# Kernel tuning notes

Measured on AMD Instinct MI355X. Metric: run time of the kernel, lower is better.

The kernel has to match this reference:

```python
import jax, jax.numpy as jnp
import numpy as np

B, C, D, H, W = 8, 256, 128, 64, 64


def setup_inputs() -> dict:
    key = jax.random.key(0)
    ks = jax.random.split(key, 7)
    s = 1.0 / np.sqrt(C)
    return {
        "q": jax.random.normal(ks[0], (B, C, H, W), dtype=jnp.float32),
        "k": jax.random.normal(ks[1], (B, C, H, W), dtype=jnp.float32),
        "v": jax.random.normal(ks[2], (B, C, H, W), dtype=jnp.float32),
        "W_theta": jax.random.normal(ks[3], (D, C), dtype=jnp.float32) * s,
        "W_phi": jax.random.normal(ks[4], (D, C), dtype=jnp.float32) * s,
        "W_g": jax.random.normal(ks[5], (D, C), dtype=jnp.float32) * s,
        "W_out": jax.random.normal(ks[6], (C, D), dtype=jnp.float32) * (1.0 / np.sqrt(D)),
    }


def reference(q, k, v, W_theta, W_phi, W_g, W_out):
    # 1x1 conv projections (no bias) == channel matmuls
    b, c, h, w = q.shape
    d = W_theta.shape[0]
    n = h * w
    qp = jnp.einsum('bchw,dc->bhwd', q, W_theta).reshape(b, n, d)   # [B,N,d]
    kp = jnp.einsum('bchw,dc->bhwd', k, W_phi).reshape(b, n, d)     # [B,N,d]
    vp = jnp.einsum('bchw,dc->bhwd', v, W_g).reshape(b, n, d)       # [B,N,d]
    # embedded_gaussian: scores / sqrt(d), softmax over dim=1 (query axis!)
    scores = jnp.einsum('bnd,bmd->bnm', qp, kp) / jnp.sqrt(jnp.asarray(d, qp.dtype))
    attn = jax.nn.softmax(scores, axis=1)                           # NOTE: axis=1, matches torch dim=1
    out = jnp.einsum('bnm,bmd->bnd', attn, vp).reshape(b, h, w, d)  # [B,H,W,d]
    out = jnp.einsum('bhwd,cd->bchw', out, W_out)                   # conv_out 1x1
    return v + out
```

## Files before the change

### kernel.cpp

```cpp
#include <hip/hip_runtime.h>
#include <stdint.h>

#define B_ 8
#define C_ 256
#define D_ 128
#define N_ 4096

typedef __bf16 bf16x8 __attribute__((ext_vector_type(8)));
typedef uint16_t u16x8 __attribute__((ext_vector_type(8)));
typedef uint16_t u16x4 __attribute__((ext_vector_type(4)));
typedef float f32x4 __attribute__((ext_vector_type(4)));

__device__ inline uint16_t f2bf(float x) {
    union { float f; uint32_t u; } v; v.f = x;
    uint32_t u = v.u;
    return (uint16_t)((u + 0x7FFFu + ((u >> 16) & 1u)) >> 16);
}

__device__ inline float dexp2(float x) { return __builtin_amdgcn_exp2f(x); }

__global__ __launch_bounds__(256) void prep_weights(
    const float* __restrict__ wt, const float* __restrict__ wp,
    const float* __restrict__ wg, const float* __restrict__ wo,
    uint16_t* __restrict__ bwt, uint16_t* __restrict__ bwp,
    uint16_t* __restrict__ bwg, uint16_t* __restrict__ bwo)
{
    int i = blockIdx.x * 256 + threadIdx.x;
    const float scale = 0.127517431f;
    bwt[i] = f2bf(wt[i] * scale);
    bwp[i] = f2bf(wp[i]);
    bwg[i] = f2bf(wg[i]);
    bwo[i] = f2bf(wo[i]);
}

__global__ __launch_bounds__(256) void proj_kernel(
    const float* __restrict__ q, const float* __restrict__ k, const float* __restrict__ v,
    const uint16_t* __restrict__ bwt, const uint16_t* __restrict__ bwp, const uint16_t* __restrict__ bwg,
    uint16_t* __restrict__ qp, uint16_t* __restrict__ kp, uint16_t* __restrict__ vpT)
{
    const int which = blockIdx.z;
    const float* src = (which == 0) ? q : ((which == 1) ? k : v);
    const uint16_t* w = (which == 0) ? bwt : ((which == 1) ? bwp : bwg);
    const int b   = blockIdx.y;
    const int n0  = blockIdx.x * 64;
    const int wav = threadIdx.x >> 6;
    const int lane = threadIdx.x & 63;
    const int col = lane & 15;
    const int quad = lane >> 4;
    const int n = n0 + wav * 16 + col;

    const float* srcb = src + (size_t)b * C_ * N_;

    f32x4 acc[8];
#pragma unroll
    for (int mf = 0; mf < 8; ++mf) acc[mf] = (f32x4){0.f, 0.f, 0.f, 0.f};

    for (int kc = 0; kc < 8; ++kc) {
        const int cbase = kc * 32 + quad * 8;
        u16x8 bb;
#pragma unroll
        for (int j = 0; j < 8; ++j)
            bb[j] = f2bf(srcb[(size_t)(cbase + j) * N_ + n]);
        bf16x8 bfrag = __builtin_bit_cast(bf16x8, bb);
#pragma unroll
        for (int mf = 0; mf < 8; ++mf) {
            bf16x8 afrag = *(const bf16x8*)(w + (size_t)(mf * 16 + col) * C_ + cbase);
            acc[mf] = __builtin_amdgcn_mfma_f32_16x16x32_bf16(afrag, bfrag, acc[mf], 0, 0, 0);
        }
    }

    if (which < 2) {
        uint16_t* dst = (which == 0) ? qp : kp;
        uint16_t* base = dst + ((size_t)b * N_ + n) * D_;
#pragma unroll
        for (int mf = 0; mf < 8; ++mf) {
            u16x4 pk;
#pragma unroll
            for (int r = 0; r < 4; ++r) pk[r] = f2bf(acc[mf][r]);
            *(u16x4*)(base + mf * 16 + quad * 4) = pk;
        }
    } else {
        uint16_t* base = vpT + (size_t)b * D_ * N_;
#pragma unroll
        for (int mf = 0; mf < 8; ++mf)
#pragma unroll
            for (int r = 0; r < 4; ++r) {
                int d = mf * 16 + quad * 4 + r;
                base[(size_t)d * N_ + n] = f2bf(acc[mf][r]);
            }
    }
}

__global__ __launch_bounds__(256) void pass1_denom(
    const uint16_t* __restrict__ qp, const uint16_t* __restrict__ kp,
    float* __restrict__ inv_denom)
{
    const int b  = blockIdx.x & 7;
    const int m0 = (blockIdx.x >> 3) * 64;
    const int wav = threadIdx.x >> 6;
    const int lane = threadIdx.x & 63;
    const int col = lane & 15;
    const int quad = lane >> 4;

    const uint16_t* qpb = qp + (size_t)b * N_ * D_;
    const uint16_t* kpb = kp + (size_t)b * N_ * D_;

    bf16x8 bfr[4][4];
#pragma unroll
    for (int mf = 0; mf < 4; ++mf)
#pragma unroll
        for (int kc = 0; kc < 4; ++kc)
            bfr[mf][kc] = *(const bf16x8*)(kpb + (size_t)(m0 + mf * 16 + col) * D_ + kc * 32 + quad * 8);

    float colsum[4] = {0.f, 0.f, 0.f, 0.f};

    for (int it = 0; it < 64; ++it) {
        const int nbase = it * 64 + wav * 16;
        bf16x8 afr[4];
#pragma unroll
        for (int kc = 0; kc < 4; ++kc)
            afr[kc] = *(const bf16x8*)(qpb + (size_t)(nbase + col) * D_ + kc * 32 + quad * 8);
#pragma unroll
        for (int mf = 0; mf < 4; ++mf) {
            f32x4 acc = (f32x4){0.f, 0.f, 0.f, 0.f};
#pragma unroll
            for (int kc = 0; kc < 4; ++kc)
                acc = __builtin_amdgcn_mfma_f32_16x16x32_bf16(afr[kc], bfr[mf][kc], acc, 0, 0, 0);
#pragma unroll
            for (int r = 0; r < 4; ++r)
                colsum[mf] += dexp2(acc[r]);
        }
    }

    __shared__ float cs[4][64];
#pragma unroll
    for (int mf = 0; mf < 4; ++mf) {
        float s = colsum[mf];
        s += __shfl_down(s, 16, 64);
        s += __shfl_down(s, 32, 64);
        if (quad == 0) cs[wav][mf * 16 + col] = s;
    }
    __syncthreads();
    if (threadIdx.x < 64) {
        float s = cs[0][threadIdx.x] + cs[1][threadIdx.x] + cs[2][threadIdx.x] + cs[3][threadIdx.x];
        inv_denom[(size_t)b * N_ + m0 + threadIdx.x] = 1.0f / s;
    }
}

__global__ __launch_bounds__(256) void pass2_attn(
    const uint16_t* __restrict__ qp, const uint16_t* __restrict__ kp,
    const uint16_t* __restrict__ vpT, const float* __restrict__ inv_denom,
    uint16_t* __restrict__ obuf0, uint16_t* __restrict__ obuf1)
{
    const int b    = blockIdx.x & 7;
    const int half = (blockIdx.x >> 3) & 1;
    const int n0   = (blockIdx.x >> 4) * 64;
    const int wav = threadIdx.x >> 6;
    const int lane = threadIdx.x & 63;
    const int col = lane & 15;
    const int quad = lane >> 4;

    const uint16_t* qpb = qp + (size_t)b * N_ * D_;
    const uint16_t* kpb = kp + (size_t)b * N_ * D_;
    const uint16_t* vtb = vpT + (size_t)b * D_ * N_;
    const float* invd = inv_denom + (size_t)b * N_;

    __shared__ __align__(16) uint16_t stage[2][16 * 512];
    __shared__ __align__(16) uint16_t plds_all[4][16][40];
    uint16_t (*plds)[40] = plds_all[wav];

    const uint16_t* kp_lane = kpb + (size_t)col * D_ + quad * 8;
    const uint16_t* vt_lane = vtb + (size_t)col * N_ + quad * 8;

#define STAGE(bufidx, m0_)                                                          \
    {                                                                               \
        uint16_t* lb = &stage[bufidx][0];                                           \
        _Pragma("unroll")                                                           \
        for (int j = 0; j < 4; ++j) {                                               \
            const int fid = wav * 4 + j;                                            \
            const uint16_t* g;                                                      \
            if (fid < 8)                                                            \
                g = kp_lane + (size_t)((m0_) + (fid >> 2) * 16) * D_ + (fid & 3) * 32; \
            else                                                                    \
                g = vt_lane + (size_t)((fid - 8) * 16) * N_ + (m0_);                \
            __builtin_amdgcn_global_load_lds(                                       \
                (const __attribute__((address_space(1))) unsigned int*)g,           \
                (__attribute__((address_space(3))) unsigned int*)(lb + fid * 512),  \
                16, 0, 0);                                                          \
        }                                                                           \
    }

    const int nrow = n0 + wav * 16 + col;
    bf16x8 qfr[4];
#pragma unroll
    for (int kc = 0; kc < 4; ++kc)
        qfr[kc] = *(const bf16x8*)(qpb + (size_t)nrow * D_ + kc * 32 + quad * 8);

    f32x4 oacc[8];
#pragma unroll
    for (int df = 0; df < 8; ++df) oacc[df] = (f32x4){0.f, 0.f, 0.f, 0.f};

    const int mstart = half * (N_ / 2);
    STAGE(0, mstart);
    __syncthreads();

    for (int chunk = 0; chunk < (N_ / 2) / 32; ++chunk) {
        const int m0 = mstart + chunk * 32;
        const int cur = chunk & 1;
        STAGE(cur ^ 1, (m0 + 32) & (N_ - 1));

        const uint16_t* sb = &stage[cur][0];
        f32x4 sacc0 = (f32x4){0.f, 0.f, 0.f, 0.f};
        f32x4 sacc1 = (f32x4){0.f, 0.f, 0.f, 0.f};
#pragma unroll
        for (int kc = 0; kc < 4; ++kc) {
            bf16x8 b0 = *(const bf16x8*)(sb + (size_t)kc * 512 + lane * 8);
            sacc0 = __builtin_amdgcn_mfma_f32_16x16x32_bf16(qfr[kc], b0, sacc0, 0, 0, 0);
        }
#pragma unroll
        for (int kc = 0; kc < 4; ++kc) {
            bf16x8 b1 = *(const bf16x8*)(sb + (size_t)(4 + kc) * 512 + lane * 8);
            sacc1 = __builtin_amdgcn_mfma_f32_16x16x32_bf16(qfr[kc], b1, sacc1, 0, 0, 0);
        }
        const float inv0 = invd[m0 + col];
        const float inv1 = invd[m0 + 16 + col];
#pragma unroll
        for (int r = 0; r < 4; ++r) {
            plds[quad * 4 + r][col]      = f2bf(dexp2(sacc0[r]) * inv0);
            plds[quad * 4 + r][16 + col] = f2bf(dexp2(sacc1[r]) * inv1);
        }
        bf16x8 pfrag = *(const bf16x8*)&plds[col][quad * 8];
#pragma unroll
        for (int df = 0; df < 8; ++df) {
            bf16x8 vfr = *(const bf16x8*)(sb + (size_t)(8 + df) * 512 + lane * 8);
            oacc[df] = __builtin_amdgcn_mfma_f32_16x16x32_bf16(pfrag, vfr, oacc[df], 0, 0, 0);
        }
        __syncthreads();
    }
#undef STAGE

    uint16_t* obufH = half ? obuf1 : obuf0;
    uint16_t* ob = obufH + ((size_t)b * N_ + n0 + wav * 16) * D_;
#pragma unroll
    for (int df = 0; df < 8; ++df)
#pragma unroll
        for (int r = 0; r < 4; ++r)
            ob[(size_t)(quad * 4 + r) * D_ + df * 16 + col] = f2bf(oacc[df][r]);
}

__global__ __launch_bounds__(256) void pass3_out(
    const uint16_t* __restrict__ obuf0, const uint16_t* __restrict__ obuf1,
    const uint16_t* __restrict__ bwo,
    const float* __restrict__ v, float* __restrict__ out)
{
    const int b  = blockIdx.y;
    const int n0 = blockIdx.x * 64;
    const int wav = threadIdx.x >> 6;
    const int lane = threadIdx.x & 63;
    const int col = lane & 15;
    const int quad = lane >> 4;
    const int n = n0 + wav * 16 + col;

    const uint16_t* ob0 = obuf0 + (size_t)b * N_ * D_;
    const uint16_t* ob1 = obuf1 + (size_t)b * N_ * D_;
    const float* vb = v + (size_t)b * C_ * N_;
    float* outb = out + (size_t)b * C_ * N_;

    bf16x8 bfr0[4], bfr1[4];
#pragma unroll
    for (int kc = 0; kc < 4; ++kc) {
        bfr0[kc] = *(const bf16x8*)(ob0 + (size_t)n * D_ + kc * 32 + quad * 8);
        bfr1[kc] = *(const bf16x8*)(ob1 + (size_t)n * D_ + kc * 32 + quad * 8);
    }

#pragma unroll
    for (int cf = 0; cf < 16; ++cf) {
        f32x4 acc = (f32x4){0.f, 0.f, 0.f, 0.f};
#pragma unroll
        for (int kc = 0; kc < 4; ++kc) {
            bf16x8 afr = *(const bf16x8*)(bwo + (size_t)(cf * 16 + col) * D_ + kc * 32 + quad * 8);
            acc = __builtin_amdgcn_mfma_f32_16x16x32_bf16(afr, bfr0[kc], acc, 0, 0, 0);
            acc = __builtin_amdgcn_mfma_f32_16x16x32_bf16(afr, bfr1[kc], acc, 0, 0, 0);
        }
#pragma unroll
        for (int r = 0; r < 4; ++r) {
            const int c = cf * 16 + quad * 4 + r;
            const size_t idx = (size_t)c * N_ + n;
            outb[idx] = vb[idx] + acc[r];
        }
    }
}

extern "C" void kernel_launch(void* const* d_in, const int* in_sizes, int n_in,
                              void* d_out, int out_size, void* d_ws, size_t ws_size,
                              hipStream_t stream) {
    const float* q  = (const float*)d_in[0];
    const float* k  = (const float*)d_in[1];
    const float* v  = (const float*)d_in[2];
    const float* wt = (const float*)d_in[3];
    const float* wp = (const float*)d_in[4];
    const float* wg = (const float*)d_in[5];
    const float* wo = (const float*)d_in[6];
    float* out = (float*)d_out;

    const size_t PROJ = (size_t)B_ * N_ * D_;
    uint16_t* qp    = (uint16_t*)d_ws;
    uint16_t* kp    = qp + PROJ;
    uint16_t* vpT   = kp + PROJ;
    uint16_t* obuf0 = vpT + PROJ;
    uint16_t* bwt   = obuf0 + PROJ;
    uint16_t* bwp   = bwt + (size_t)D_ * C_;
    uint16_t* bwg   = bwp + (size_t)D_ * C_;
    uint16_t* bwo   = bwg + (size_t)D_ * C_;
    float* invd     = (float*)(bwo + (size_t)D_ * C_);
    uint16_t* obuf1 = (uint16_t*)(invd + (size_t)B_ * N_);

    prep_weights<<<dim3(128), 256, 0, stream>>>(wt, wp, wg, wo, bwt, bwp, bwg, bwo);
    proj_kernel<<<dim3(N_ / 64, B_, 3), 256, 0, stream>>>(q, k, v, bwt, bwp, bwg, qp, kp, vpT);
    pass1_denom<<<dim3(512), 256, 0, stream>>>(qp, kp, invd);
    pass2_attn<<<dim3(1024), 256, 0, stream>>>(qp, kp, vpT, invd, obuf0, obuf1);
    pass3_out<<<dim3(N_ / 64, B_), 256, 0, stream>>>(obuf0, obuf1, bwo, v, out);
}
```

Before: 428.4 us.

## Fold softmax denominator into V and retile attention with larger per-wave query tiles

Pass1 now scales the transposed V projection in place by the per-key inverse denominator, so pass2 no longer loads or multiplies by inv_denom. Pass2 is restructured: each wave owns 64 query rows and the key axis is split into quarters. K and V fragments are loaded straight from global memory instead of being staged through LDS with barriers, and the P tile is written with packed bf16 stores. Setprio hints are added around the MFMA blocks. The trade-offs are more register pressure (launch bounds of 2), four partial output buffers read by pass3, an extra bf16 rounding of V, and pass1 now runs on twice as many blocks with 32 keys each, which lengthens its critical path.

After: 466.2 us. +8.8%, slower.

```diff
diff --git a/kernel.cpp b/kernel.cpp
--- a/kernel.cpp
+++ b/kernel.cpp
@@ -10,11 +10,23 @@
 typedef uint16_t u16x8 __attribute__((ext_vector_type(8)));
 typedef uint16_t u16x4 __attribute__((ext_vector_type(4)));
 typedef float f32x4 __attribute__((ext_vector_type(4)));
+typedef uint32_t u32x2 __attribute__((ext_vector_type(2)));
 
 __device__ inline uint16_t f2bf(float x) {
     union { float f; uint32_t u; } v; v.f = x;
     uint32_t u = v.u;
     return (uint16_t)((u + 0x7FFFu + ((u >> 16) & 1u)) >> 16);
+}
+
+__device__ inline float bf2f(uint16_t v) {
+    union { uint32_t u; float f; } x; x.u = (uint32_t)v << 16; return x.f;
+}
+
+__device__ inline uint32_t pkbf(float lo, float hi) {
+    __bf16 l = (__bf16)lo, h = (__bf16)hi;
+    uint16_t lu = __builtin_bit_cast(uint16_t, l);
+    uint16_t hu = __builtin_bit_cast(uint16_t, h);
+    return ((uint32_t)hu << 16) | (uint32_t)lu;
 }
 
 __device__ inline float dexp2(float x) { return __builtin_amdgcn_exp2f(x); }
@@ -93,35 +105,35 @@
 
 __global__ __launch_bounds__(256) void pass1_denom(
     const uint16_t* __restrict__ qp, const uint16_t* __restrict__ kp,
-    float* __restrict__ inv_denom)
+    uint16_t* __restrict__ vpT)
 {
     const int b  = blockIdx.x & 7;
-    const int m0 = (blockIdx.x >> 3) * 64;
+    const int m0 = (blockIdx.x >> 3) * 32;
     const int wav = threadIdx.x >> 6;
     const int lane = threadIdx.x & 63;
-    const int col = lane & 15;
-    const int quad = lane >> 4;
+    const int c = lane & 15;
+    const int q = lane >> 4;
 
     const uint16_t* qpb = qp + (size_t)b * N_ * D_;
     const uint16_t* kpb = kp + (size_t)b * N_ * D_;
 
-    bf16x8 bfr[4][4];
-#pragma unroll
-    for (int mf = 0; mf < 4; ++mf)
+    bf16x8 bfr[2][4];
+#pragma unroll
+    for (int mf = 0; mf < 2; ++mf)
 #pragma unroll
         for (int kc = 0; kc < 4; ++kc)
-            bfr[mf][kc] = *(const bf16x8*)(kpb + (size_t)(m0 + mf * 16 + col) * D_ + kc * 32 + quad * 8);
-
-    float colsum[4] = {0.f, 0.f, 0.f, 0.f};
+            bfr[mf][kc] = *(const bf16x8*)(kpb + (size_t)(m0 + mf * 16 + c) * D_ + kc * 32 + q * 8);
+
+    float colsum[2] = {0.f, 0.f};
 
     for (int it = 0; it < 64; ++it) {
         const int nbase = it * 64 + wav * 16;
         bf16x8 afr[4];
 #pragma unroll
         for (int kc = 0; kc < 4; ++kc)
-            afr[kc] = *(const bf16x8*)(qpb + (size_t)(nbase + col) * D_ + kc * 32 + quad * 8);
-#pragma unroll
-        for (int mf = 0; mf < 4; ++mf) {
+            afr[kc] = *(const bf16x8*)(qpb + (size_t)(nbase + c) * D_ + kc * 32 + q * 8);
+#pragma unroll
+        for (int mf = 0; mf < 2; ++mf) {
             f32x4 acc = (f32x4){0.f, 0.f, 0.f, 0.f};
 #pragma unroll
             for (int kc = 0; kc < 4; ++kc)
@@ -132,124 +144,131 @@
         }
     }
 
-    __shared__ float cs[4][64];
-#pragma unroll
-    for (int mf = 0; mf < 4; ++mf) {
+    __shared__ float cs[4][32];
+    __shared__ float sinv[32];
+#pragma unroll
+    for (int mf = 0; mf < 2; ++mf) {
         float s = colsum[mf];
         s += __shfl_down(s, 16, 64);
         s += __shfl_down(s, 32, 64);
-        if (quad == 0) cs[wav][mf * 16 + col] = s;
+        if (q == 0) cs[wav][mf * 16 + c] = s;
     }
     __syncthreads();
-    if (threadIdx.x < 64) {
+    if (threadIdx.x < 32) {
         float s = cs[0][threadIdx.x] + cs[1][threadIdx.x] + cs[2][threadIdx.x] + cs[3][threadIdx.x];
-        inv_denom[(size_t)b * N_ + m0 + threadIdx.x] = 1.0f / s;
-    }
-}
-
-__global__ __launch_bounds__(256) void pass2_attn(
+        sinv[threadIdx.x] = 1.0f / s;
+    }
+    __syncthreads();
+    uint16_t* vtb = vpT + (size_t)b * D_ * N_;
+#pragma unroll
+    for (int j = 0; j < 16; ++j) {
+        int e = threadIdx.x + j * 256;
+        int d = e >> 5, m = e & 31;
+        size_t idx = (size_t)d * N_ + m0 + m;
+        vtb[idx] = f2bf(bf2f(vtb[idx]) * sinv[m]);
+    }
+}
+
+__global__ __launch_bounds__(256, 2) void pass2_attn(
     const uint16_t* __restrict__ qp, const uint16_t* __restrict__ kp,
-    const uint16_t* __restrict__ vpT, const float* __restrict__ inv_denom,
-    uint16_t* __restrict__ obuf0, uint16_t* __restrict__ obuf1)
-{
-    const int b    = blockIdx.x & 7;
-    const int half = (blockIdx.x >> 3) & 1;
-    const int n0   = (blockIdx.x >> 4) * 64;
+    const uint16_t* __restrict__ vpT,
+    uint16_t* __restrict__ ob0, uint16_t* __restrict__ ob1,
+    uint16_t* __restrict__ ob2, uint16_t* __restrict__ ob3)
+{
+    const int b   = blockIdx.x & 7;
+    const int qtr = (blockIdx.x >> 3) & 3;
+    const int nsb = blockIdx.x >> 5;
     const int wav = threadIdx.x >> 6;
     const int lane = threadIdx.x & 63;
-    const int col = lane & 15;
-    const int quad = lane >> 4;
+    const int c = lane & 15;
+    const int q = lane >> 4;
+    const int ntile = nsb * 256 + wav * 64;
 
     const uint16_t* qpb = qp + (size_t)b * N_ * D_;
     const uint16_t* kpb = kp + (size_t)b * N_ * D_;
     const uint16_t* vtb = vpT + (size_t)b * D_ * N_;
-    const float* invd = inv_denom + (size_t)b * N_;
-
-    __shared__ __align__(16) uint16_t stage[2][16 * 512];
-    __shared__ __align__(16) uint16_t plds_all[4][16][40];
-    uint16_t (*plds)[40] = plds_all[wav];
-
-    const uint16_t* kp_lane = kpb + (size_t)col * D_ + quad * 8;
-    const uint16_t* vt_lane = vtb + (size_t)col * N_ + quad * 8;
-
-#define STAGE(bufidx, m0_)                                                          \
-    {                                                                               \
-        uint16_t* lb = &stage[bufidx][0];                                           \
-        _Pragma("unroll")                                                           \
-        for (int j = 0; j < 4; ++j) {                                               \
-            const int fid = wav * 4 + j;                                            \
-            const uint16_t* g;                                                      \
-            if (fid < 8)                                                            \
-                g = kp_lane + (size_t)((m0_) + (fid >> 2) * 16) * D_ + (fid & 3) * 32; \
-            else                                                                    \
-                g = vt_lane + (size_t)((fid - 8) * 16) * N_ + (m0_);                \
-            __builtin_amdgcn_global_load_lds(                                       \
-                (const __attribute__((address_space(1))) unsigned int*)g,           \
-                (__attribute__((address_space(3))) unsigned int*)(lb + fid * 512),  \
-                16, 0, 0);                                                          \
-        }                                                                           \
-    }
-
-    const int nrow = n0 + wav * 16 + col;
-    bf16x8 qfr[4];
-#pragma unroll
-    for (int kc = 0; kc < 4; ++kc)
-        qfr[kc] = *(const bf16x8*)(qpb + (size_t)nrow * D_ + kc * 32 + quad * 8);
-
-    f32x4 oacc[8];
-#pragma unroll
-    for (int df = 0; df < 8; ++df) oacc[df] = (f32x4){0.f, 0.f, 0.f, 0.f};
-
-    const int mstart = half * (N_ / 2);
-    STAGE(0, mstart);
-    __syncthreads();
-
-    for (int chunk = 0; chunk < (N_ / 2) / 32; ++chunk) {
-        const int m0 = mstart + chunk * 32;
-        const int cur = chunk & 1;
-        STAGE(cur ^ 1, (m0 + 32) & (N_ - 1));
-
-        const uint16_t* sb = &stage[cur][0];
-        f32x4 sacc0 = (f32x4){0.f, 0.f, 0.f, 0.f};
-        f32x4 sacc1 = (f32x4){0.f, 0.f, 0.f, 0.f};
-#pragma unroll
-        for (int kc = 0; kc < 4; ++kc) {
-            bf16x8 b0 = *(const bf16x8*)(sb + (size_t)kc * 512 + lane * 8);
-            sacc0 = __builtin_amdgcn_mfma_f32_16x16x32_bf16(qfr[kc], b0, sacc0, 0, 0, 0);
-        }
-#pragma unroll
-        for (int kc = 0; kc < 4; ++kc) {
-            bf16x8 b1 = *(const bf16x8*)(sb + (size_t)(4 + kc) * 512 + lane * 8);
-            sacc1 = __builtin_amdgcn_mfma_f32_16x16x32_bf16(qfr[kc], b1, sacc1, 0, 0, 0);
-        }
-        const float inv0 = invd[m0 + col];
-        const float inv1 = invd[m0 + 16 + col];
-#pragma unroll
-        for (int r = 0; r < 4; ++r) {
-            plds[quad * 4 + r][col]      = f2bf(dexp2(sacc0[r]) * inv0);
-            plds[quad * 4 + r][16 + col] = f2bf(dexp2(sacc1[r]) * inv1);
-        }
-        bf16x8 pfrag = *(const bf16x8*)&plds[col][quad * 8];
-#pragma unroll
-        for (int df = 0; df < 8; ++df) {
-            bf16x8 vfr = *(const bf16x8*)(sb + (size_t)(8 + df) * 512 + lane * 8);
-            oacc[df] = __builtin_amdgcn_mfma_f32_16x16x32_bf16(pfrag, vfr, oacc[df], 0, 0, 0);
-        }
-        __syncthreads();
-    }
-#undef STAGE
-
-    uint16_t* obufH = half ? obuf1 : obuf0;
-    uint16_t* ob = obufH + ((size_t)b * N_ + n0 + wav * 16) * D_;
-#pragma unroll
-    for (int df = 0; df < 8; ++df)
-#pragma unroll
-        for (int r = 0; r < 4; ++r)
-            ob[(size_t)(quad * 4 + r) * D_ + df * 16 + col] = f2bf(oacc[df][r]);
+
+    __shared__ __align__(16) uint16_t plds[4][4][16][72];
+
+    bf16x8 qfr[4][4];
+#pragma unroll
+    for (int nf = 0; nf < 4; ++nf)
+#pragma unroll
+        for (int kc = 0; kc < 4; ++kc)
+            qfr[nf][kc] = *(const bf16x8*)(qpb + (size_t)(ntile + nf * 16 + c) * D_ + kc * 32 + q * 8);
+
+    f32x4 oacc[4][8];
+#pragma unroll
+    for (int nf = 0; nf < 4; ++nf)
+#pragma unroll
+        for (int df = 0; df < 8; ++df) oacc[nf][df] = (f32x4){0.f, 0.f, 0.f, 0.f};
+
+    const int mstart = qtr * (N_ / 4);
+    for (int ch = 0; ch < (N_ / 4) / 32; ++ch) {
+        const int m0 = mstart + ch * 32;
+
+        bf16x8 kf[2][4];
+#pragma unroll
+        for (int mf = 0; mf < 2; ++mf)
+#pragma unroll
+            for (int kc = 0; kc < 4; ++kc)
+                kf[mf][kc] = *(const bf16x8*)(kpb + (size_t)(m0 + mf * 16 + c) * D_ + kc * 32 + q * 8);
+
+        __builtin_amdgcn_s_setprio(1);
+#pragma unroll
+        for (int nf = 0; nf < 4; ++nf) {
+            f32x4 s0 = (f32x4){0.f, 0.f, 0.f, 0.f};
+            f32x4 s1 = (f32x4){0.f, 0.f, 0.f, 0.f};
+#pragma unroll
+            for (int kc = 0; kc < 4; ++kc)
+                s0 = __builtin_amdgcn_mfma_f32_16x16x32_bf16(kf[0][kc], qfr[nf][kc], s0, 0, 0, 0);
+#pragma unroll
+            for (int kc = 0; kc < 4; ++kc)
+                s1 = __builtin_amdgcn_mfma_f32_16x16x32_bf16(kf[1][kc], qfr[nf][kc], s1, 0, 0, 0);
+            uint32_t p00 = pkbf(dexp2(s0[0]), dexp2(s0[1]));
+            uint32_t p01 = pkbf(dexp2(s0[2]), dexp2(s0[3]));
+            uint32_t p10 = pkbf(dexp2(s1[0]), dexp2(s1[1]));
+            uint32_t p11 = pkbf(dexp2(s1[2]), dexp2(s1[3]));
+            uint16_t* row = &plds[wav][nf][c][0];
+            *(u32x2*)(row + 4 * q)      = (u32x2){p00, p01};
+            *(u32x2*)(row + 16 + 4 * q) = (u32x2){p10, p11};
+        }
+        __builtin_amdgcn_s_setprio(0);
+
+        bf16x8 vf[8];
+#pragma unroll
+        for (int df = 0; df < 8; ++df)
+            vf[df] = *(const bf16x8*)(vtb + (size_t)(df * 16 + c) * N_ + m0 + q * 8);
+
+        bf16x8 pf[4];
+#pragma unroll
+        for (int nf = 0; nf < 4; ++nf)
+            pf[nf] = *(const bf16x8*)(&plds[wav][nf][c][8 * q]);
+
+        __builtin_amdgcn_s_setprio(1);
+#pragma unroll
+        for (int nf = 0; nf < 4; ++nf)
+#pragma unroll
+            for (int df = 0; df < 8; ++df)
+                oacc[nf][df] = __builtin_amdgcn_mfma_f32_16x16x32_bf16(pf[nf], vf[df], oacc[nf][df], 0, 0, 0);
+        __builtin_amdgcn_s_setprio(0);
+    }
+
+    uint16_t* obq = (qtr == 0) ? ob0 : (qtr == 1) ? ob1 : (qtr == 2) ? ob2 : ob3;
+#pragma unroll
+    for (int nf = 0; nf < 4; ++nf) {
+        uint16_t* ob = obq + ((size_t)b * N_ + ntile + nf * 16) * D_;
+#pragma unroll
+        for (int df = 0; df < 8; ++df)
+#pragma unroll
+            for (int r = 0; r < 4; ++r)
+                ob[(size_t)(q * 4 + r) * D_ + df * 16 + c] = f2bf(oacc[nf][df][r]);
+    }
 }
 
 __global__ __launch_bounds__(256) void pass3_out(
-    const uint16_t* __restrict__ obuf0, const uint16_t* __restrict__ obuf1,
+    const uint16_t* __restrict__ ob0, const uint16_t* __restrict__ ob1,
+    const uint16_t* __restrict__ ob2, const uint16_t* __restrict__ ob3,
     const uint16_t* __restrict__ bwo,
     const float* __restrict__ v, float* __restrict__ out)
 {
@@ -261,16 +280,17 @@
     const int quad = lane >> 4;
     const int n = n0 + wav * 16 + col;
 
-    const uint16_t* ob0 = obuf0 + (size_t)b * N_ * D_;
-    const uint16_t* ob1 = obuf1 + (size_t)b * N_ * D_;
     const float* vb = v + (size_t)b * C_ * N_;
     float* outb = out + (size_t)b * C_ * N_;
-
-    bf16x8 bfr0[4], bfr1[4];
+    const size_t off = ((size_t)b * N_ + n) * D_;
+
+    bf16x8 f0[4], f1[4], f2[4], f3[4];
 #pragma unroll
     for (int kc = 0; kc < 4; ++kc) {
-        bfr0[kc] = *(const bf16x8*)(ob0 + (size_t)n * D_ + kc * 32 + quad * 8);
-        bfr1[kc] = *(const bf16x8*)(ob1 + (size_t)n * D_ + kc * 32 + quad * 8);
+        f0[kc] = *(const bf16x8*)(ob0 + off + kc * 32 + quad * 8);
+        f1[kc] = *(const bf16x8*)(ob1 + off + kc * 32 + quad * 8);
+        f2[kc] = *(const bf16x8*)(ob2 + off + kc * 32 + quad * 8);
+        f3[kc] = *(const bf16x8*)(ob3 + off + kc * 32 + quad * 8);
     }
 
 #pragma unroll
@@ -279,13 +299,15 @@
 #pragma unroll
         for (int kc = 0; kc < 4; ++kc) {
             bf16x8 afr = *(const bf16x8*)(bwo + (size_t)(cf * 16 + col) * D_ + kc * 32 + quad * 8);
-            acc = __builtin_amdgcn_mfma_f32_16x16x32_bf16(afr, bfr0[kc], acc, 0, 0, 0);
-            acc = __builtin_amdgcn_mfma_f32_16x16x32_bf16(afr, bfr1[kc], acc, 0, 0, 0);
+            acc = __builtin_amdgcn_mfma_f32_16x16x32_bf16(afr, f0[kc], acc, 0, 0, 0);
+            acc = __builtin_amdgcn_mfma_f32_16x16x32_bf16(afr, f1[kc], acc, 0, 0, 0);
+            acc = __builtin_amdgcn_mfma_f32_16x16x32_bf16(afr, f2[kc], acc, 0, 0, 0);
+            acc = __builtin_amdgcn_mfma_f32_16x16x32_bf16(afr, f3[kc], acc, 0, 0, 0);
         }
 #pragma unroll
         for (int r = 0; r < 4; ++r) {
-            const int c = cf * 16 + quad * 4 + r;
-            const size_t idx = (size_t)c * N_ + n;
+            const int cc = cf * 16 + quad * 4 + r;
+            const size_t idx = (size_t)cc * N_ + n;
             outb[idx] = vb[idx] + acc[r];
         }
     }
@@ -304,20 +326,21 @@
     float* out = (float*)d_out;
 
     const size_t PROJ = (size_t)B_ * N_ * D_;
-    uint16_t* qp    = (uint16_t*)d_ws;
-    uint16_t* kp    = qp + PROJ;
-    uint16_t* vpT   = kp + PROJ;
-    uint16_t* obuf0 = vpT + PROJ;
-    uint16_t* bwt   = obuf0 + PROJ;
-    uint16_t* bwp   = bwt + (size_t)D_ * C_;
-    uint16_t* bwg   = bwp + (size_t)D_ * C_;
-    uint16_t* bwo   = bwg + (size_t)D_ * C_;
-    float* invd     = (float*)(bwo + (size_t)D_ * C_);
-    uint16_t* obuf1 = (uint16_t*)(invd + (size_t)B_ * N_);
+    uint16_t* qp  = (uint16_t*)d_ws;
+    uint16_t* kp  = qp + PROJ;
+    uint16_t* vpT = kp + PROJ;
+    uint16_t* ob0 = vpT + PROJ;
+    uint16_t* ob1 = ob0 + PROJ;
+    uint16_t* ob2 = ob1 + PROJ;
+    uint16_t* ob3 = ob2 + PROJ;
+    uint16_t* bwt = ob3 + PROJ;
+    uint16_t* bwp = bwt + (size_t)D_ * C_;
+    uint16_t* bwg = bwp + (size_t)D_ * C_;
+    uint16_t* bwo = bwg + (size_t)D_ * C_;
 
     prep_weights<<<dim3(128), 256, 0, stream>>>(wt, wp, wg, wo, bwt, bwp, bwg, bwo);
     proj_kernel<<<dim3(N_ / 64, B_, 3), 256, 0, stream>>>(q, k, v, bwt, bwp, bwg, qp, kp, vpT);
-    pass1_denom<<<dim3(512), 256, 0, stream>>>(qp, kp, invd);
-    pass2_attn<<<dim3(1024), 256, 0, stream>>>(qp, kp, vpT, invd, obuf0, obuf1);
-    pass3_out<<<dim3(N_ / 64, B_), 256, 0, stream>>>(obuf0, obuf1, bwo, v, out);
-}
+    pass1_denom<<<dim3(1024), 256, 0, stream>>>(qp, kp, vpT);
+    pass2_attn<<<dim3(512), 256, 0, stream>>>(qp, kp, vpT, ob0, ob1, ob2, ob3);
+    pass3_out<<<dim3(N_ / 64, B_), 256, 0, stream>>>(ob0, ob1, ob2, ob3, bwo, v, out);
+}
```
